# Optimization experiments

Hardware: AMD Instinct MI355X
Metric: run time of the kernel (lower is better)

The kernel has to match this reference:

```python
import jax, jax.numpy as jnp
import numpy as np

N = 262144        # 64^3 grid unknowns
NNZ = 7 * N       # ~7-point stencil sparsity
BS = 32


def setup_inputs() -> dict:
    key = jax.random.key(0)
    k1, k2, k3, k4, k5 = jax.random.split(key, 5)
    y_pred = jax.random.normal(k1, (BS, N), dtype=jnp.float32)
    y_true = jax.random.normal(k2, (BS, N), dtype=jnp.float32)
    A_vals = jax.random.normal(k3, (NNZ,), dtype=jnp.float32)
    A_rows = jax.random.randint(k4, (NNZ,), 0, N, dtype=jnp.int32)
    A_cols = jax.random.randint(k5, (NNZ,), 0, N, dtype=jnp.int32)
    return {"y_pred": y_pred, "y_true": y_true, "A_vals": A_vals,
            "A_rows": A_rows, "A_cols": A_cols}


def reference(y_pred, y_true, A_vals, A_rows, A_cols):
    # YhatY[b] = <y_true[b], y_pred[b]>
    YhatY = jnp.sum(y_true * y_pred, axis=1)                      # (bs,)
    # Sparse matvec per batch: YhatAt = (A @ y_pred.T).T, COO form.
    # gathered[e, b] = A_vals[e] * y_pred[b, A_cols[e]]
    gathered = (y_pred[:, A_cols] * A_vals).T                     # (nnz, bs)
    YhatAt = jax.ops.segment_sum(gathered, A_rows, num_segments=N).T  # (bs, N)
    # YhatYhatAt[b] = <y_pred[b], A y_pred[b]>
    YhatYhatAt = jnp.sum(y_pred * YhatAt, axis=1)                 # (bs,)
    # diag(YhatY / YhatYhatAt) @ YhatAt == row-wise scale by alpha
    alpha = YhatY / YhatYhatAt                                    # (bs,)
    resid = y_true - alpha[:, None] * YhatAt                      # (bs, N)
    return jnp.mean(jnp.sum(resid * resid, axis=1))
```

## Files before the change

kernel.cpp:

```cpp
#include <hip/hip_runtime.h>

#define NGRID 262144
#define NNZ_C 1835008
#define BSZ   32

__device__ __forceinline__ float block_reduce_sum_256(float v) {
    __shared__ float red[4];
    #pragma unroll
    for (int o = 32; o > 0; o >>= 1) v += __shfl_down(v, o);
    const int wave = threadIdx.x >> 6;
    const int lane = threadIdx.x & 63;
    if (lane == 0) red[wave] = v;
    __syncthreads();
    float s = 0.f;
    if (threadIdx.x == 0) {
        #pragma unroll
        for (int i = 0; i < 4; ++i) s += red[i];
    }
    return s;
}

__global__ void k_transpose_zero(const float* __restrict__ yp,
                                 float* __restrict__ yp_t,
                                 float* __restrict__ yat_t) {
    __shared__ float tile[64 * 33];
    const int tid = threadIdx.x;
    const size_t n0 = (size_t)blockIdx.x * 64;
    const int lane_n = tid & 63;
    const int bq = tid >> 6;
    #pragma unroll
    for (int r = 0; r < 8; ++r) {
        const int b = bq * 8 + r;
        tile[lane_n * 33 + b] = yp[(size_t)b * NGRID + n0 + lane_n];
    }
    __syncthreads();
    #pragma unroll
    for (int w = 0; w < 8; ++w) {
        const int f = w * 256 + tid;
        yp_t[n0 * 32 + f] = tile[(f >> 5) * 33 + (f & 31)];
        yat_t[n0 * 32 + f] = 0.f;
    }
}

__global__ void k_scatter(const float* __restrict__ vals,
                          const int* __restrict__ rows,
                          const int* __restrict__ cols,
                          const float* __restrict__ yp_t,
                          float* __restrict__ yat_t) {
    const size_t tid = (size_t)blockIdx.x * blockDim.x + threadIdx.x;
    const int b = (int)(tid & 31);
    const size_t e = tid >> 5;
    const float v = vals[e];
    const int r = rows[e];
    const int c = cols[e];
    const float x = yp_t[(size_t)c * 32 + b];
    atomicAdd(&yat_t[(size_t)r * 32 + b], v * x);
}

__global__ void k_dot_yty(const float* __restrict__ yt,
                          const float* __restrict__ yp,
                          float* __restrict__ p1) {
    const int b = blockIdx.y;
    const float4* yt4 = (const float4*)(yt + (size_t)b * NGRID);
    const float4* yp4 = (const float4*)(yp + (size_t)b * NGRID);
    float acc = 0.f;
    for (int i = blockIdx.x * 256 + threadIdx.x; i < NGRID / 4; i += 64 * 256) {
        const float4 a = yt4[i];
        const float4 c = yp4[i];
        acc = fmaf(a.x, c.x, acc);
        acc = fmaf(a.y, c.y, acc);
        acc = fmaf(a.z, c.z, acc);
        acc = fmaf(a.w, c.w, acc);
    }
    const float s = block_reduce_sum_256(acc);
    if (threadIdx.x == 0) p1[b * 64 + blockIdx.x] = s;
}

__global__ void k_dot_yyat(const float* __restrict__ yp_t,
                           const float* __restrict__ yat_t,
                           float* __restrict__ p2) {
    __shared__ float lds[1024];
    float acc[4] = {0.f, 0.f, 0.f, 0.f};
    const float4* a4 = (const float4*)yp_t;
    const float4* b4 = (const float4*)yat_t;
    for (int i = blockIdx.x * 256 + threadIdx.x; i < (NGRID * 32) / 4; i += 256 * 256) {
        const float4 a = a4[i];
        const float4 b = b4[i];
        acc[0] = fmaf(a.x, b.x, acc[0]);
        acc[1] = fmaf(a.y, b.y, acc[1]);
        acc[2] = fmaf(a.z, b.z, acc[2]);
        acc[3] = fmaf(a.w, b.w, acc[3]);
    }
    #pragma unroll
    for (int j = 0; j < 4; ++j) lds[threadIdx.x * 4 + j] = acc[j];
    __syncthreads();
    if (threadIdx.x < 32) {
        float s = 0.f;
        for (int k = 0; k < 32; ++k) s += lds[threadIdx.x + 32 * k];
        p2[blockIdx.x * 32 + threadIdx.x] = s;
    }
}

__global__ void k_alpha(const float* __restrict__ p1,
                        const float* __restrict__ p2,
                        float* __restrict__ alpha) {
    const int b = threadIdx.x;
    float s1 = 0.f, s2 = 0.f;
    for (int j = 0; j < 64; ++j) s1 += p1[b * 64 + j];
    for (int k = 0; k < 256; ++k) s2 += p2[k * 32 + b];
    alpha[b] = s1 / s2;
}

__global__ void k_loss(const float* __restrict__ yt,
                       const float* __restrict__ yat_t,
                       const float* __restrict__ alpha,
                       float* __restrict__ p3) {
    __shared__ float tile[256 * 33];
    __shared__ float a_sh[32];
    const int tid = threadIdx.x;
    if (tid < 32) a_sh[tid] = alpha[tid];
    const size_t n0 = (size_t)blockIdx.x * 256;
    #pragma unroll
    for (int w = 0; w < 32; ++w) {
        const int f = w * 256 + tid;
        tile[(f >> 5) * 33 + (f & 31)] = yat_t[n0 * 32 + f];
    }
    __syncthreads();
    const int wave = tid >> 6;
    const int lane = tid & 63;
    float acc = 0.f;
    #pragma unroll
    for (int j = 0; j < 8; ++j) {
        const int b = wave * 8 + j;
        const float a = a_sh[b];
        const float* ytr = yt + (size_t)b * NGRID + n0;
        #pragma unroll
        for (int c = 0; c < 4; ++c) {
            const int nl = c * 64 + lane;
            const float t = ytr[nl];
            const float yv = tile[nl * 33 + b];
            const float r = fmaf(-a, yv, t);
            acc = fmaf(r, r, acc);
        }
    }
    const float s = block_reduce_sum_256(acc);
    if (tid == 0) p3[blockIdx.x] = s;
}

__global__ void k_final(const float* __restrict__ p3, float* __restrict__ out) {
    float acc = 0.f;
    for (int i = threadIdx.x; i < 1024; i += 256) acc += p3[i];
    const float s = block_reduce_sum_256(acc);
    if (threadIdx.x == 0) out[0] = s * (1.0f / 32.0f);
}

extern "C" void kernel_launch(void* const* d_in, const int* in_sizes, int n_in,
                              void* d_out, int out_size, void* d_ws, size_t ws_size,
                              hipStream_t stream) {
    const float* yp = (const float*)d_in[0];
    const float* yt = (const float*)d_in[1];
    const float* Av = (const float*)d_in[2];
    const int*   Ar = (const int*)d_in[3];
    const int*   Ac = (const int*)d_in[4];
    float* out = (float*)d_out;

    float* ws    = (float*)d_ws;
    float* yp_t  = ws;
    float* yat_t = yp_t + (size_t)NGRID * 32;
    float* p1    = yat_t + (size_t)NGRID * 32;
    float* p2    = p1 + 32 * 64;
    float* alpha = p2 + 256 * 32;
    float* p3    = alpha + 32;

    k_transpose_zero<<<NGRID / 64, 256, 0, stream>>>(yp, yp_t, yat_t);
    k_scatter<<<(NNZ_C * 32) / 256, 256, 0, stream>>>(Av, Ar, Ac, yp_t, yat_t);
    k_dot_yty<<<dim3(64, 32), 256, 0, stream>>>(yt, yp, p1);
    k_dot_yyat<<<256, 256, 0, stream>>>(yp_t, yat_t, p2);
    k_alpha<<<1, 32, 0, stream>>>(p1, p2, alpha);
    k_loss<<<NGRID / 256, 256, 0, stream>>>(yt, yat_t, alpha, p3);
    k_final<<<1, 256, 0, stream>>>(p3, out);
}
```

Before: 358.1 us.

## Bucket-sort COO entries by row block and accumulate SpMM in LDS

Replaces the global-atomic COO scatter with a counting sort of nonzeros into 1024 row buckets (histogram, scan, reorder), then accumulates each 256-row bucket in shared memory with LDS atomics. It fuses the y_true·y_pred dot into the transpose pass and the y_pred·(A y_pred) dot into the accumulate pass, and drops the zeroing of the yat buffer. The aim is to remove the 59M device-memory atomics and the separate reduction passes. In exchange it adds sort kernels that re-read the index arrays several times, needs a larger workspace (it falls back to the old path if the workspace is too small), and can suffer load imbalance if buckets are uneven.

Result: slower. 698.3 us (+95.0%).

```diff
diff --git a/kernel.cpp b/kernel.cpp
--- a/kernel.cpp
+++ b/kernel.cpp
@@ -2,7 +2,8 @@
 
 #define NGRID 262144
 #define NNZ_C 1835008
-#define BSZ   32
+#define NBKT  1024
+#define BROWS 256
 
 __device__ __forceinline__ float block_reduce_sum_256(float v) {
     __shared__ float red[4];
@@ -18,6 +19,219 @@
         for (int i = 0; i < 4; ++i) s += red[i];
     }
     return s;
+}
+
+
+__global__ __launch_bounds__(256) void k_prep(
+        const float* __restrict__ yp, const float* __restrict__ yt,
+        float* __restrict__ yp_t, float* __restrict__ p1,
+        int* __restrict__ hist) {
+    __shared__ float tile[64 * 33];
+    const int tid = threadIdx.x;
+    if (blockIdx.x == 0) {
+        #pragma unroll
+        for (int i = 0; i < 4; ++i) hist[i * 256 + tid] = 0;
+    }
+    const size_t n0 = (size_t)blockIdx.x * 64;
+    const int lane = tid & 63;
+    const int w = tid >> 6;
+    float acc[8];
+    #pragma unroll
+    for (int r = 0; r < 8; ++r) {
+        const int b = w * 8 + r;
+        const float a = yp[(size_t)b * NGRID + n0 + lane];
+        const float t = yt[(size_t)b * NGRID + n0 + lane];
+        tile[lane * 33 + b] = a;
+        acc[r] = a * t;
+    }
+    __syncthreads();
+    #pragma unroll
+    for (int q = 0; q < 8; ++q) {
+        const int f = q * 256 + tid;
+        yp_t[n0 * 32 + f] = tile[(f >> 5) * 33 + (f & 31)];
+    }
+    #pragma unroll
+    for (int r = 0; r < 8; ++r) {
+        float v = acc[r];
+        #pragma unroll
+        for (int o = 32; o > 0; o >>= 1) v += __shfl_down(v, o);
+        if (lane == 0) p1[blockIdx.x * 32 + w * 8 + r] = v;
+    }
+}
+
+__global__ __launch_bounds__(256) void k_hist(const int* __restrict__ rows,
+                                              int* __restrict__ hist) {
+    __shared__ int h[NBKT];
+    const int tid = threadIdx.x;
+    for (int i = tid; i < NBKT; i += 256) h[i] = 0;
+    __syncthreads();
+    const int chunk = NNZ_C / 512;
+    const size_t e0 = (size_t)blockIdx.x * chunk;
+    for (int i = tid; i < chunk; i += 256) atomicAdd(&h[rows[e0 + i] >> 8], 1);
+    __syncthreads();
+    for (int i = tid; i < NBKT; i += 256)
+        if (h[i]) atomicAdd(&hist[i], h[i]);
+}
+
+__global__ __launch_bounds__(1024) void k_scan(const int* __restrict__ hist,
+                                               int* __restrict__ base,
+                                               int* __restrict__ cursor) {
+    __shared__ int s[2][NBKT];
+    const int tid = threadIdx.x;
+    const int v = hist[tid];
+    s[0][tid] = v;
+    __syncthreads();
+    int p = 0;
+    for (int off = 1; off < NBKT; off <<= 1) {
+        int t = s[p][tid];
+        if (tid >= off) t += s[p][tid - off];
+        s[1 ^ p][tid] = t;
+        __syncthreads();
+        p ^= 1;
+    }
+    const int excl = s[p][tid] - v;
+    base[tid] = excl;
+    cursor[tid] = excl;
+    if (tid == 0) base[NBKT] = NNZ_C;
+}
+
+__global__ __launch_bounds__(256) void k_reorder(
+        const int* __restrict__ rows, const int* __restrict__ cols,
+        const float* __restrict__ vals, int* __restrict__ cursor,
+        int* __restrict__ rc_out, float* __restrict__ v_out) {
+    __shared__ int h[NBKT];
+    __shared__ int bl[NBKT];
+    const int tid = threadIdx.x;
+    for (int i = tid; i < NBKT; i += 256) h[i] = 0;
+    __syncthreads();
+    const int chunk = NNZ_C / 256;
+    const size_t e0 = (size_t)blockIdx.x * chunk;
+    for (int i = tid; i < chunk; i += 256) atomicAdd(&h[rows[e0 + i] >> 8], 1);
+    __syncthreads();
+    for (int i = tid; i < NBKT; i += 256) {
+        const int c = h[i];
+        bl[i] = c ? atomicAdd(&cursor[i], c) : 0;
+        h[i] = 0;
+    }
+    __syncthreads();
+    for (int i = tid; i < chunk; i += 256) {
+        const int r = rows[e0 + i];
+        const int bk = r >> 8;
+        const int off = atomicAdd(&h[bk], 1);
+        const int pos = bl[bk] + off;
+        rc_out[pos] = ((r & 255) << 24) | cols[e0 + i];
+        v_out[pos] = vals[e0 + i];
+    }
+}
+
+__global__ __launch_bounds__(256) void k_accum(
+        const int* __restrict__ rc, const float* __restrict__ vv,
+        const int* __restrict__ base, const float* __restrict__ yp_t,
+        float* __restrict__ yat_t, float* __restrict__ p2) {
+    __shared__ float acc[BROWS * 32];
+    __shared__ float red[256];
+    const int tid = threadIdx.x;
+    #pragma unroll
+    for (int i = 0; i < 32; ++i) acc[i * 256 + tid] = 0.f;
+    __syncthreads();
+    const int k = blockIdx.x;
+    const int start = base[k], end = base[k + 1];
+    const int half = tid >> 5;
+    const int b = tid & 31;
+    for (int e = start + half; e < end; e += 16) {
+        const int e1 = e + 8;
+        const bool has1 = (e1 < end);
+        const int rc0 = rc[e];
+        const float v0 = vv[e];
+        int rc1 = 0; float v1 = 0.f;
+        if (has1) { rc1 = rc[e1]; v1 = vv[e1]; }
+        const float x0 = yp_t[(size_t)(rc0 & 0x3FFFF) * 32 + b];
+        float x1 = 0.f;
+        if (has1) x1 = yp_t[(size_t)(rc1 & 0x3FFFF) * 32 + b];
+        atomicAdd(&acc[(((unsigned)rc0) >> 24) * 32 + b], v0 * x0);
+        if (has1) atomicAdd(&acc[(((unsigned)rc1) >> 24) * 32 + b], v1 * x1);
+    }
+    __syncthreads();
+    const size_t o0 = (size_t)k * (BROWS * 32);
+    float pa = 0.f;
+    #pragma unroll
+    for (int i = 0; i < 32; ++i) {
+        const int f = i * 256 + tid;
+        const float a = acc[f];
+        pa = fmaf(a, yp_t[o0 + f], pa);
+        yat_t[o0 + f] = a;
+    }
+    red[tid] = pa;
+    __syncthreads();
+    if (tid < 32) {
+        float s = 0.f;
+        #pragma unroll
+        for (int j = 0; j < 8; ++j) s += red[tid + 32 * j];
+        p2[k * 32 + tid] = s;
+    }
+}
+
+__global__ __launch_bounds__(256) void k_alpha2(const float* __restrict__ p1,
+                                                const float* __restrict__ p2,
+                                                float* __restrict__ alpha) {
+    __shared__ float r1[256], r2[256];
+    const int tid = threadIdx.x;
+    const int b = tid & 31, j = tid >> 5;
+    float s1 = 0.f, s2 = 0.f;
+    for (int k = j; k < 4096; k += 8) s1 += p1[k * 32 + b];
+    for (int k = j; k < NBKT; k += 8) s2 += p2[k * 32 + b];
+    r1[tid] = s1; r2[tid] = s2;
+    __syncthreads();
+    if (tid < 32) {
+        float a = 0.f, c = 0.f;
+        #pragma unroll
+        for (int q = 0; q < 8; ++q) { a += r1[tid + 32 * q]; c += r2[tid + 32 * q]; }
+        alpha[tid] = a / c;
+    }
+}
+
+
+__global__ __launch_bounds__(256) void k_loss(
+        const float* __restrict__ yt, const float* __restrict__ yat_t,
+        const float* __restrict__ alpha, float* __restrict__ p3) {
+    __shared__ float tile[256 * 33];
+    __shared__ float a_sh[32];
+    const int tid = threadIdx.x;
+    if (tid < 32) a_sh[tid] = alpha[tid];
+    const size_t n0 = (size_t)blockIdx.x * 256;
+    #pragma unroll
+    for (int w = 0; w < 32; ++w) {
+        const int f = w * 256 + tid;
+        tile[(f >> 5) * 33 + (f & 31)] = yat_t[n0 * 32 + f];
+    }
+    __syncthreads();
+    const int wave = tid >> 6;
+    const int lane = tid & 63;
+    float acc = 0.f;
+    #pragma unroll
+    for (int j = 0; j < 8; ++j) {
+        const int b = wave * 8 + j;
+        const float a = a_sh[b];
+        const float* ytr = yt + (size_t)b * NGRID + n0;
+        #pragma unroll
+        for (int c = 0; c < 4; ++c) {
+            const int nl = c * 64 + lane;
+            const float t = ytr[nl];
+            const float yv = tile[nl * 33 + b];
+            const float r = fmaf(-a, yv, t);
+            acc = fmaf(r, r, acc);
+        }
+    }
+    const float s = block_reduce_sum_256(acc);
+    if (tid == 0) p3[blockIdx.x] = s;
+}
+
+__global__ __launch_bounds__(256) void k_final(const float* __restrict__ p3,
+                                               float* __restrict__ out) {
+    float acc = 0.f;
+    for (int i = threadIdx.x; i < 1024; i += 256) acc += p3[i];
+    const float s = block_reduce_sum_256(acc);
+    if (threadIdx.x == 0) out[0] = s * (1.0f / 32.0f);
 }
 
 __global__ void k_transpose_zero(const float* __restrict__ yp,
@@ -101,57 +315,14 @@
     }
 }
 
-__global__ void k_alpha(const float* __restrict__ p1,
-                        const float* __restrict__ p2,
-                        float* __restrict__ alpha) {
+__global__ void k_alpha_old(const float* __restrict__ p1,
+                            const float* __restrict__ p2,
+                            float* __restrict__ alpha) {
     const int b = threadIdx.x;
     float s1 = 0.f, s2 = 0.f;
     for (int j = 0; j < 64; ++j) s1 += p1[b * 64 + j];
     for (int k = 0; k < 256; ++k) s2 += p2[k * 32 + b];
     alpha[b] = s1 / s2;
-}
-
-__global__ void k_loss(const float* __restrict__ yt,
-                       const float* __restrict__ yat_t,
-                       const float* __restrict__ alpha,
-                       float* __restrict__ p3) {
-    __shared__ float tile[256 * 33];
-    __shared__ float a_sh[32];
-    const int tid = threadIdx.x;
-    if (tid < 32) a_sh[tid] = alpha[tid];
-    const size_t n0 = (size_t)blockIdx.x * 256;
-    #pragma unroll
-    for (int w = 0; w < 32; ++w) {
-        const int f = w * 256 + tid;
-        tile[(f >> 5) * 33 + (f & 31)] = yat_t[n0 * 32 + f];
-    }
-    __syncthreads();
-    const int wave = tid >> 6;
-    const int lane = tid & 63;
-    float acc = 0.f;
-    #pragma unroll
-    for (int j = 0; j < 8; ++j) {
-        const int b = wave * 8 + j;
-        const float a = a_sh[b];
-        const float* ytr = yt + (size_t)b * NGRID + n0;
-        #pragma unroll
-        for (int c = 0; c < 4; ++c) {
-            const int nl = c * 64 + lane;
-            const float t = ytr[nl];
-            const float yv = tile[nl * 33 + b];
-            const float r = fmaf(-a, yv, t);
-            acc = fmaf(r, r, acc);
-        }
-    }
-    const float s = block_reduce_sum_256(acc);
-    if (tid == 0) p3[blockIdx.x] = s;
-}
-
-__global__ void k_final(const float* __restrict__ p3, float* __restrict__ out) {
-    float acc = 0.f;
-    for (int i = threadIdx.x; i < 1024; i += 256) acc += p3[i];
-    const float s = block_reduce_sum_256(acc);
-    if (threadIdx.x == 0) out[0] = s * (1.0f / 32.0f);
 }
 
 extern "C" void kernel_launch(void* const* d_in, const int* in_sizes, int n_in,
@@ -164,19 +335,40 @@
     const int*   Ac = (const int*)d_in[4];
     float* out = (float*)d_out;
 
-    float* ws    = (float*)d_ws;
-    float* yp_t  = ws;
-    float* yat_t = yp_t + (size_t)NGRID * 32;
-    float* p1    = yat_t + (size_t)NGRID * 32;
-    float* p2    = p1 + 32 * 64;
-    float* alpha = p2 + 256 * 32;
-    float* p3    = alpha + 32;
-
-    k_transpose_zero<<<NGRID / 64, 256, 0, stream>>>(yp, yp_t, yat_t);
-    k_scatter<<<(NNZ_C * 32) / 256, 256, 0, stream>>>(Av, Ar, Ac, yp_t, yat_t);
-    k_dot_yty<<<dim3(64, 32), 256, 0, stream>>>(yt, yp, p1);
-    k_dot_yyat<<<256, 256, 0, stream>>>(yp_t, yat_t, p2);
-    k_alpha<<<1, 32, 0, stream>>>(p1, p2, alpha);
-    k_loss<<<NGRID / 256, 256, 0, stream>>>(yt, yat_t, alpha, p3);
-    k_final<<<1, 256, 0, stream>>>(p3, out);
-}
+    float* ws     = (float*)d_ws;
+    float* yp_t   = ws;
+    float* yat_t  = yp_t + (size_t)NGRID * 32;
+    int*   rc     = (int*)(yat_t + (size_t)NGRID * 32);
+    float* vv     = (float*)(rc + NNZ_C);
+    int*   hist   = (int*)(vv + NNZ_C);
+    int*   basep  = hist + NBKT;
+    int*   cursor = basep + NBKT + 1;
+    float* p1     = (float*)(cursor + NBKT);
+    float* p2     = p1 + 4096 * 32;
+    float* alpha  = p2 + NBKT * 32;
+    float* p3     = alpha + 32;
+    const size_t need = (size_t)(p3 + 1024 - ws) * sizeof(float);
+
+    if (ws_size >= need) {
+        k_prep<<<NGRID / 64, 256, 0, stream>>>(yp, yt, yp_t, p1, hist);
+        k_hist<<<512, 256, 0, stream>>>(Ar, hist);
+        k_scan<<<1, 1024, 0, stream>>>(hist, basep, cursor);
+        k_reorder<<<256, 256, 0, stream>>>(Ar, Ac, Av, cursor, rc, vv);
+        k_accum<<<NBKT, 256, 0, stream>>>(rc, vv, basep, yp_t, yat_t, p2);
+        k_alpha2<<<1, 256, 0, stream>>>(p1, p2, alpha);
+        k_loss<<<NGRID / 256, 256, 0, stream>>>(yt, yat_t, alpha, p3);
+        k_final<<<1, 256, 0, stream>>>(p3, out);
+    } else {
+        float* f_p1    = (float*)(yat_t + (size_t)NGRID * 32);
+        float* f_p2    = f_p1 + 32 * 64;
+        float* f_alpha = f_p2 + 256 * 32;
+        float* f_p3    = f_alpha + 32;
+        k_transpose_zero<<<NGRID / 64, 256, 0, stream>>>(yp, yp_t, yat_t);
+        k_scatter<<<(NNZ_C * 32) / 256, 256, 0, stream>>>(Av, Ar, Ac, yp_t, yat_t);
+        k_dot_yty<<<dim3(64, 32), 256, 0, stream>>>(yt, yp, f_p1);
+        k_dot_yyat<<<256, 256, 0, stream>>>(yp_t, yat_t, f_p2);
+        k_alpha_old<<<1, 32, 0, stream>>>(f_p1, f_p2, f_alpha);
+        k_loss<<<NGRID / 256, 256, 0, stream>>>(yt, yat_t, f_alpha, f_p3);
+        k_final<<<1, 256, 0, stream>>>(f_p3, out);
+    }
+}
```

## Expand squared residual algebraically and fuse reductions into prep and post passes

Applied to the files above, without the earlier changes.

The loss is expanded as tt - 2a*c2 + a^2*c3, so alpha no longer has to be known before the residual pass. The y_true·y_pred dot is folded into the transpose kernel, and one post kernel computes all per-batch sums, accumulating them with atomics into a small buffer. A tiny finisher then combines them. This cuts the kernel count from seven to four and avoids rereading y_pred and y_true in separate dot kernels, at the cost of float atomics and possible cancellation in the expanded form.

After: 551.4 us. 1.54x slower.

```diff
diff --git a/kernel.cpp b/kernel.cpp
--- a/kernel.cpp
+++ b/kernel.cpp
@@ -2,43 +2,40 @@
 
 #define NGRID 262144
 #define NNZ_C 1835008
-#define BSZ   32
 
-__device__ __forceinline__ float block_reduce_sum_256(float v) {
-    __shared__ float red[4];
-    #pragma unroll
-    for (int o = 32; o > 0; o >>= 1) v += __shfl_down(v, o);
-    const int wave = threadIdx.x >> 6;
-    const int lane = threadIdx.x & 63;
-    if (lane == 0) red[wave] = v;
-    __syncthreads();
-    float s = 0.f;
-    if (threadIdx.x == 0) {
-        #pragma unroll
-        for (int i = 0; i < 4; ++i) s += red[i];
-    }
-    return s;
-}
 
-__global__ void k_transpose_zero(const float* __restrict__ yp,
-                                 float* __restrict__ yp_t,
-                                 float* __restrict__ yat_t) {
+__global__ __launch_bounds__(256) void k_prep(
+        const float* __restrict__ yp, const float* __restrict__ yt,
+        float* __restrict__ yp_t, float* __restrict__ yat_t,
+        float* __restrict__ p1, float* __restrict__ S) {
     __shared__ float tile[64 * 33];
     const int tid = threadIdx.x;
+    if (blockIdx.x == 0 && tid < 160) S[tid] = 0.f;
     const size_t n0 = (size_t)blockIdx.x * 64;
-    const int lane_n = tid & 63;
-    const int bq = tid >> 6;
+    const int lane = tid & 63;
+    const int w = tid >> 6;
+    float acc[8];
     #pragma unroll
     for (int r = 0; r < 8; ++r) {
-        const int b = bq * 8 + r;
-        tile[lane_n * 33 + b] = yp[(size_t)b * NGRID + n0 + lane_n];
+        const int b = w * 8 + r;
+        const float a = yp[(size_t)b * NGRID + n0 + lane];
+        const float t = yt[(size_t)b * NGRID + n0 + lane];
+        tile[lane * 33 + b] = a;
+        acc[r] = a * t;
     }
     __syncthreads();
     #pragma unroll
-    for (int w = 0; w < 8; ++w) {
-        const int f = w * 256 + tid;
+    for (int q = 0; q < 8; ++q) {
+        const int f = q * 256 + tid;
         yp_t[n0 * 32 + f] = tile[(f >> 5) * 33 + (f & 31)];
         yat_t[n0 * 32 + f] = 0.f;
+    }
+    #pragma unroll
+    for (int r = 0; r < 8; ++r) {
+        float v = acc[r];
+        #pragma unroll
+        for (int o = 32; o > 0; o >>= 1) v += __shfl_down(v, o);
+        if (lane == 0) p1[blockIdx.x * 32 + w * 8 + r] = v;
     }
 }
 
@@ -57,101 +54,91 @@
     atomicAdd(&yat_t[(size_t)r * 32 + b], v * x);
 }
 
-__global__ void k_dot_yty(const float* __restrict__ yt,
-                          const float* __restrict__ yp,
-                          float* __restrict__ p1) {
-    const int b = blockIdx.y;
-    const float4* yt4 = (const float4*)(yt + (size_t)b * NGRID);
-    const float4* yp4 = (const float4*)(yp + (size_t)b * NGRID);
-    float acc = 0.f;
-    for (int i = blockIdx.x * 256 + threadIdx.x; i < NGRID / 4; i += 64 * 256) {
-        const float4 a = yt4[i];
-        const float4 c = yp4[i];
-        acc = fmaf(a.x, c.x, acc);
-        acc = fmaf(a.y, c.y, acc);
-        acc = fmaf(a.z, c.z, acc);
-        acc = fmaf(a.w, c.w, acc);
+__global__ __launch_bounds__(256) void k_post(
+        const float* __restrict__ yat_t, const float* __restrict__ yp_t,
+        const float* __restrict__ yt, const float* __restrict__ p1,
+        float* __restrict__ S) {
+    __shared__ float tile[256 * 33];
+    __shared__ float red[2][256];
+    __shared__ float redp[128];
+    const int tid = threadIdx.x;
+    const size_t n0 = (size_t)blockIdx.x * 256;
+
+    if (tid < 128) redp[tid] = p1[blockIdx.x * 128 + tid];
+
+    float c1 = 0.f, c3 = 0.f;
+    #pragma unroll
+    for (int i = 0; i < 32; ++i) {
+        const int f = i * 256 + tid;
+        const float a = yat_t[n0 * 32 + f];
+        const float p = yp_t[n0 * 32 + f];
+        c1 = fmaf(p, a, c1);
+        c3 = fmaf(a, a, c3);
+        tile[(f >> 5) * 33 + (f & 31)] = a;
     }
-    const float s = block_reduce_sum_256(acc);
-    if (threadIdx.x == 0) p1[b * 64 + blockIdx.x] = s;
-}
+    red[0][tid] = c1;
+    red[1][tid] = c3;
+    __syncthreads();
 
-__global__ void k_dot_yyat(const float* __restrict__ yp_t,
-                           const float* __restrict__ yat_t,
-                           float* __restrict__ p2) {
-    __shared__ float lds[1024];
-    float acc[4] = {0.f, 0.f, 0.f, 0.f};
-    const float4* a4 = (const float4*)yp_t;
-    const float4* b4 = (const float4*)yat_t;
-    for (int i = blockIdx.x * 256 + threadIdx.x; i < (NGRID * 32) / 4; i += 256 * 256) {
-        const float4 a = a4[i];
-        const float4 b = b4[i];
-        acc[0] = fmaf(a.x, b.x, acc[0]);
-        acc[1] = fmaf(a.y, b.y, acc[1]);
-        acc[2] = fmaf(a.z, b.z, acc[2]);
-        acc[3] = fmaf(a.w, b.w, acc[3]);
-    }
-    #pragma unroll
-    for (int j = 0; j < 4; ++j) lds[threadIdx.x * 4 + j] = acc[j];
-    __syncthreads();
-    if (threadIdx.x < 32) {
-        float s = 0.f;
-        for (int k = 0; k < 32; ++k) s += lds[threadIdx.x + 32 * k];
-        p2[blockIdx.x * 32 + threadIdx.x] = s;
-    }
-}
-
-__global__ void k_alpha(const float* __restrict__ p1,
-                        const float* __restrict__ p2,
-                        float* __restrict__ alpha) {
-    const int b = threadIdx.x;
-    float s1 = 0.f, s2 = 0.f;
-    for (int j = 0; j < 64; ++j) s1 += p1[b * 64 + j];
-    for (int k = 0; k < 256; ++k) s2 += p2[k * 32 + b];
-    alpha[b] = s1 / s2;
-}
-
-__global__ void k_loss(const float* __restrict__ yt,
-                       const float* __restrict__ yat_t,
-                       const float* __restrict__ alpha,
-                       float* __restrict__ p3) {
-    __shared__ float tile[256 * 33];
-    __shared__ float a_sh[32];
-    const int tid = threadIdx.x;
-    if (tid < 32) a_sh[tid] = alpha[tid];
-    const size_t n0 = (size_t)blockIdx.x * 256;
-    #pragma unroll
-    for (int w = 0; w < 32; ++w) {
-        const int f = w * 256 + tid;
-        tile[(f >> 5) * 33 + (f & 31)] = yat_t[n0 * 32 + f];
-    }
-    __syncthreads();
-    const int wave = tid >> 6;
+    const int w = tid >> 6;
     const int lane = tid & 63;
-    float acc = 0.f;
     #pragma unroll
     for (int j = 0; j < 8; ++j) {
-        const int b = wave * 8 + j;
-        const float a = a_sh[b];
+        const int b = w * 8 + j;
         const float* ytr = yt + (size_t)b * NGRID + n0;
+        float c2 = 0.f, tt = 0.f;
         #pragma unroll
         for (int c = 0; c < 4; ++c) {
             const int nl = c * 64 + lane;
             const float t = ytr[nl];
             const float yv = tile[nl * 33 + b];
-            const float r = fmaf(-a, yv, t);
-            acc = fmaf(r, r, acc);
+            c2 = fmaf(t, yv, c2);
+            tt = fmaf(t, t, tt);
+        }
+        #pragma unroll
+        for (int o = 32; o > 0; o >>= 1) {
+            c2 += __shfl_down(c2, o);
+            tt += __shfl_down(tt, o);
+        }
+        if (lane == 0) {
+            atomicAdd(&S[32 + b], c2);
+            atomicAdd(&S[96 + b], tt);
         }
     }
-    const float s = block_reduce_sum_256(acc);
-    if (tid == 0) p3[blockIdx.x] = s;
+
+    if (tid < 32) {
+        float s1 = 0.f, s3 = 0.f;
+        #pragma unroll
+        for (int k = 0; k < 8; ++k) {
+            s1 += red[0][tid + 32 * k];
+            s3 += red[1][tid + 32 * k];
+        }
+        float sy = redp[tid] + redp[tid + 32] + redp[tid + 64] + redp[tid + 96];
+        atomicAdd(&S[0 + tid], s1);
+        atomicAdd(&S[64 + tid], s3);
+        atomicAdd(&S[128 + tid], sy);
+    }
 }
 
-__global__ void k_final(const float* __restrict__ p3, float* __restrict__ out) {
-    float acc = 0.f;
-    for (int i = threadIdx.x; i < 1024; i += 256) acc += p3[i];
-    const float s = block_reduce_sum_256(acc);
-    if (threadIdx.x == 0) out[0] = s * (1.0f / 32.0f);
+__global__ void k_finish(const float* __restrict__ S, float* __restrict__ out) {
+    __shared__ float lb[32];
+    const int tid = threadIdx.x;
+    if (tid < 32) {
+        const float c1 = S[tid];
+        const float c2 = S[32 + tid];
+        const float c3 = S[64 + tid];
+        const float tt = S[96 + tid];
+        const float ty = S[128 + tid];
+        const float a = ty / c1;
+        lb[tid] = fmaf(a * a, c3, fmaf(-2.f * a, c2, tt));
+    }
+    __syncthreads();
+    if (tid == 0) {
+        float s = 0.f;
+        #pragma unroll
+        for (int i = 0; i < 32; ++i) s += lb[i];
+        out[0] = s * (1.0f / 32.0f);
+    }
 }
 
 extern "C" void kernel_launch(void* const* d_in, const int* in_sizes, int n_in,
@@ -168,15 +155,10 @@
     float* yp_t  = ws;
     float* yat_t = yp_t + (size_t)NGRID * 32;
     float* p1    = yat_t + (size_t)NGRID * 32;
-    float* p2    = p1 + 32 * 64;
-    float* alpha = p2 + 256 * 32;
-    float* p3    = alpha + 32;
+    float* S     = p1 + 4096 * 32;
 
-    k_transpose_zero<<<NGRID / 64, 256, 0, stream>>>(yp, yp_t, yat_t);
+    k_prep<<<NGRID / 64, 256, 0, stream>>>(yp, yt, yp_t, yat_t, p1, S);
     k_scatter<<<(NNZ_C * 32) / 256, 256, 0, stream>>>(Av, Ar, Ac, yp_t, yat_t);
-    k_dot_yty<<<dim3(64, 32), 256, 0, stream>>>(yt, yp, p1);
-    k_dot_yyat<<<256, 256, 0, stream>>>(yp_t, yat_t, p2);
-    k_alpha<<<1, 32, 0, stream>>>(p1, p2, alpha);
-    k_loss<<<NGRID / 256, 256, 0, stream>>>(yt, yat_t, alpha, p3);
-    k_final<<<1, 256, 0, stream>>>(p3, out);
+    k_post<<<NGRID / 256, 256, 0, stream>>>(yat_t, yp_t, yt, p1, S);
+    k_finish<<<1, 64, 0, stream>>>(S, out);
 }
```
